# Performance work log

Measured on AMD Instinct MI355X. Metric: run time of the kernel, lower is better.

Reference implementation:

```python
import jax, jax.numpy as jnp
import numpy as np
import math

B, QL, HID = 1, 512, 4096
NH, NKV, HD = 32, 8, 128
PAST = 3584
THETA = 10000.0
GS = 32            # group_size for both K (k_bits=4 -> stays 32) and V
KBITS = 4
VBITS = 4
KRR = 0.125        # k_residual_ratio
VRR = 0.125        # v_residual_ratio


def qdq(x, g, bits):
    # asymmetric per-group quantize->dequantize along last dim (KVmix quantize_pack + dequant gemm)
    shp = x.shape
    xg = x.reshape(shp[:-1] + (shp[-1] // g, g))
    mn = xg.min(-1, keepdims=True)
    mx = xg.max(-1, keepdims=True)
    qmax = float(2 ** bits - 1)
    scale = (mx - mn) / qmax
    q = jnp.clip(jnp.round(jnp.where(scale > 0, (xg - mn) / jnp.where(scale > 0, scale, 1.0), 0.0)), 0.0, qmax)
    return (q * scale + mn).reshape(shp)


def _rope(x, cos, sin):
    h = x.shape[-1] // 2
    rot = jnp.concatenate([-x[..., h:], x[..., :h]], -1)
    return x * cos + rot * sin


def setup_inputs() -> dict:
    key = jax.random.key(0)
    ks = jax.random.split(key, 7)
    s = 0.02
    return {
        "hidden_states": jax.random.normal(ks[0], (B, QL, HID), jnp.float32),
        "past_key": jax.random.normal(ks[1], (B, NKV, PAST, HD), jnp.float32),
        "past_value": jax.random.normal(ks[2], (B, NKV, PAST, HD), jnp.float32),
        "wq": jax.random.normal(ks[3], (NH * HD, HID), jnp.float32) * s,
        "wk": jax.random.normal(ks[4], (NKV * HD, HID), jnp.float32) * s,
        "wv": jax.random.normal(ks[5], (NKV * HD, HID), jnp.float32) * s,
        "wo": jax.random.normal(ks[6], (HID, NH * HD), jnp.float32) * s,
        "position_ids": (jnp.arange(QL, dtype=jnp.int32) + PAST)[None, :],
    }


def reference(hidden_states, past_key, past_value, wq, wk, wv, wo, position_ids):
    b, ql, _ = hidden_states.shape
    past_len = past_key.shape[2]
    kv_len = past_len + ql

    # projections -> [b, heads, seq, hd]
    q = (hidden_states @ wq.T).reshape(b, ql, NH, HD).transpose(0, 2, 1, 3)
    k = (hidden_states @ wk.T).reshape(b, ql, NKV, HD).transpose(0, 2, 1, 3)
    v = (hidden_states @ wv.T).reshape(b, ql, NKV, HD).transpose(0, 2, 1, 3)

    # rotary embedding (HF Mistral style)
    inv_freq = 1.0 / (THETA ** (jnp.arange(0, HD, 2, dtype=jnp.float32) / HD))
    freqs = position_ids.astype(jnp.float32)[..., None] * inv_freq       # [b, ql, hd/2]
    emb = jnp.concatenate([freqs, freqs], -1)                            # [b, ql, hd]
    cos = jnp.cos(emb)[:, None]
    sin = jnp.sin(emb)[:, None]
    q = _rope(q, cos, sin)
    k = _rope(k, cos, sin)

    key_full = jnp.concatenate([past_key, k], axis=2)                    # [b, nkv, kv, hd]
    val_full = jnp.concatenate([past_value, v], axis=2)

    # residual split (static python ints)
    k_res = int(KRR * kv_len)
    kq_len = (kv_len - k_res) // GS * GS
    v_res = int(VRR * kv_len)
    vq_len = (kv_len - v_res) // GS * GS

    # K quantized along seq dim (transpose(2,3) then group last dim), V along head_dim
    key_q = qdq(key_full[:, :, :kq_len, :].transpose(0, 1, 3, 2), GS, KBITS)  # [b,nkv,hd,kq]
    key_f = key_full[:, :, kq_len:, :]
    val_q = qdq(val_full[:, :, :vq_len, :], GS, VBITS)
    val_f = val_full[:, :, vq_len:, :]

    rep = NH // NKV
    rkv = lambda x: jnp.repeat(x, rep, axis=1)

    att_q = jnp.einsum('bhqd,bhdk->bhqk', q, rkv(key_q))
    att_f = jnp.einsum('bhqd,bhkd->bhqk', q, rkv(key_f))
    attn = jnp.concatenate([att_q, att_f], -1).astype(jnp.float32) / math.sqrt(HD)

    qpos = past_len + jnp.arange(ql)
    mask = jnp.where(jnp.arange(kv_len)[None, :] <= qpos[:, None], 0.0, -1e30)
    attn = jax.nn.softmax(attn + mask, axis=-1)

    out = jnp.einsum('bhqk,bhkd->bhqd', attn[..., :vq_len], rkv(val_q)) \
        + jnp.einsum('bhqk,bhkd->bhqd', attn[..., vq_len:], rkv(val_f))
    out = out.transpose(0, 2, 1, 3).reshape(b, ql, NH * HD)
    return out @ wo.T
```

## Files before the change

kernel.cpp:

```cpp
#include <hip/hip_runtime.h>
#include <hip/hip_bf16.h>

typedef __bf16 bf16_t;
typedef __bf16 bf16x4 __attribute__((ext_vector_type(4)));
typedef __bf16 bf16x8 __attribute__((ext_vector_type(8)));
typedef float  f32x4  __attribute__((ext_vector_type(4)));

static __device__ __forceinline__ f32x4 mfma16(bf16x8 a, bf16x8 b, f32x4 c) {
  return __builtin_amdgcn_mfma_f32_16x16x32_bf16(a, b, c, 0, 0, 0);
}

typedef const __attribute__((address_space(1))) void* gas_t;
typedef __attribute__((address_space(3))) void* las_t;
#define ASYNC16(g, l) __builtin_amdgcn_global_load_lds((gas_t)(g), (las_t)(l), 16, 0, 0)

#define QL_   512
#define HID_  4096
#define NH_   32
#define NKV_  8
#define HD_   128
#define PAST_ 3584
#define KVL_  4096
#define NSPLIT 6

#define QSCALE 0.12751750152134056f

__global__ __launch_bounds__(256) void cvt_f32_bf16(
    const float* __restrict__ src, bf16_t* __restrict__ dst, int n4)
{
  int i = blockIdx.x * 256 + threadIdx.x;
  const int stride = gridDim.x * 256;
  for (; i < n4; i += stride) {
    float4 f = ((const float4*)src)[i];
    bf16x4 o;
    o[0] = (bf16_t)f.x; o[1] = (bf16_t)f.y; o[2] = (bf16_t)f.z; o[3] = (bf16_t)f.w;
    ((bf16x4*)dst)[i] = o;
  }
}

template<bool C_F32>
__global__ __launch_bounds__(256) void gemm_bt(
    const bf16_t* __restrict__ A,
    const bf16_t* __restrict__ B0, const bf16_t* __restrict__ B1,
    const bf16_t* __restrict__ B2, int nsplit1, int nsplit2,
    void* __restrict__ Cptr, int K, int lda, int ldb, int ldc)
{
  constexpr int BM = 128, BN = 64, BK = 32;
  __shared__ bf16_t As[BM * BK];
  __shared__ bf16_t Bs[BN * BK];

  const int tid = threadIdx.x;
  const int w = tid >> 6, lane = tid & 63;
  const int lm = lane & 15, quad = lane >> 4;
  const int wr = w >> 1, wc = w & 1;
  const int bm0 = blockIdx.y * BM, bn0 = blockIdx.x * BN;

  const bf16_t* Bseg; int bn_loc;
  if (bn0 < nsplit1)      { Bseg = B0; bn_loc = bn0; }
  else if (bn0 < nsplit2) { Bseg = B1; bn_loc = bn0 - nsplit1; }
  else                    { Bseg = B2; bn_loc = bn0 - nsplit2; }

  int rA[2], cA[2];
#pragma unroll
  for (int j = 0; j < 2; j++) {
    const int g = (w * 2 + j) * 64 + lane;
    rA[j] = g >> 2;
    cA[j] = (g & 3) ^ ((rA[j] >> 1) & 3);
  }
  const int gB = w * 64 + lane;
  const int rB = gB >> 2;
  const int cB = (gB & 3) ^ ((rB >> 1) & 3);

  f32x4 acc[4][2];
#pragma unroll
  for (int i = 0; i < 4; i++)
#pragma unroll
    for (int j = 0; j < 2; j++) acc[i][j] = f32x4{0.f, 0.f, 0.f, 0.f};

  const bf16_t* Abase = A + (size_t)bm0 * lda;
  const bf16_t* Bbase = Bseg + (size_t)bn_loc * ldb;

  for (int k0 = 0; k0 < K; k0 += BK) {
    ASYNC16(Abase + (size_t)rA[0] * lda + k0 + cA[0] * 8, &As[(w * 2 + 0) * 512]);
    ASYNC16(Abase + (size_t)rA[1] * lda + k0 + cA[1] * 8, &As[(w * 2 + 1) * 512]);
    ASYNC16(Bbase + (size_t)rB * ldb + k0 + cB * 8,       &Bs[w * 512]);
    __syncthreads();

    bf16x8 af[4], bfr[2];
#pragma unroll
    for (int mt = 0; mt < 4; mt++) {
      const int r = wr * 64 + mt * 16 + lm;
      af[mt] = *(const bf16x8*)&As[(r * 4 + (quad ^ ((r >> 1) & 3))) * 8];
    }
#pragma unroll
    for (int nt = 0; nt < 2; nt++) {
      const int r = wc * 32 + nt * 16 + lm;
      bfr[nt] = *(const bf16x8*)&Bs[(r * 4 + (quad ^ ((r >> 1) & 3))) * 8];
    }
#pragma unroll
    for (int mt = 0; mt < 4; mt++)
#pragma unroll
      for (int nt = 0; nt < 2; nt++)
        acc[mt][nt] = mfma16(af[mt], bfr[nt], acc[mt][nt]);
    __syncthreads();
  }

#pragma unroll
  for (int mt = 0; mt < 4; mt++) {
#pragma unroll
    for (int nt = 0; nt < 2; nt++) {
      const int row = bm0 + wr * 64 + mt * 16 + quad * 4;
      const int col = bn0 + wc * 32 + nt * 16 + lm;
#pragma unroll
      for (int r = 0; r < 4; r++) {
        if constexpr (C_F32)
          ((float*)Cptr)[(size_t)(row + r) * ldc + col] = acc[mt][nt][r];
        else
          ((bf16_t*)Cptr)[(size_t)(row + r) * ldc + col] = (bf16_t)acc[mt][nt][r];
      }
    }
  }
}

__global__ __launch_bounds__(128) void dequant_key(
    const float* __restrict__ pk, bf16_t* __restrict__ Kf)
{
  const int g = blockIdx.x, h = blockIdx.y, d = threadIdx.x;
  const float* src = pk + ((size_t)h * PAST_ + g * 32) * HD_ + d;
  float x[32];
  float mn = 1e30f, mx = -1e30f;
#pragma unroll
  for (int s = 0; s < 32; s++) {
    x[s] = src[(size_t)s * HD_];
    mn = fminf(mn, x[s]); mx = fmaxf(mx, x[s]);
  }
  float scale = (mx - mn) / 15.0f;
  bf16_t* dst = Kf + ((size_t)h * KVL_ + g * 32) * HD_ + d;
#pragma unroll
  for (int s = 0; s < 32; s++) {
    float t = scale > 0.f ? (x[s] - mn) / scale : 0.f;
    float q = fminf(fmaxf(rintf(t), 0.f), 15.f);
    dst[(size_t)s * HD_] = (bf16_t)(q * scale + mn);
  }
}

__global__ __launch_bounds__(256) void dequant_value(
    const float* __restrict__ pv, bf16_t* __restrict__ Vt)
{
  const int sc = blockIdx.x, h = blockIdx.y;
  const int j = threadIdx.x >> 6, lane = threadIdx.x & 63;
  const int s = sc * 64 + lane;
  const float* src = pv + ((size_t)h * PAST_ + s) * HD_ + j * 32;
  float x[32];
  float mn = 1e30f, mx = -1e30f;
#pragma unroll
  for (int q4 = 0; q4 < 8; q4++) {
    float4 f = ((const float4*)src)[q4];
    x[q4*4+0] = f.x; x[q4*4+1] = f.y; x[q4*4+2] = f.z; x[q4*4+3] = f.w;
    mn = fminf(fminf(mn, fminf(f.x, f.y)), fminf(f.z, f.w));
    mx = fmaxf(fmaxf(mx, fmaxf(f.x, f.y)), fmaxf(f.z, f.w));
  }
  float scale = (mx - mn) / 15.0f;
  bf16_t* dst = Vt + ((size_t)h * HD_ + j * 32) * KVL_ + s;
#pragma unroll
  for (int d = 0; d < 32; d++) {
    float t = scale > 0.f ? (x[d] - mn) / scale : 0.f;
    float q = fminf(fmaxf(rintf(t), 0.f), 15.f);
    dst[(size_t)d * KVL_] = (bf16_t)(q * scale + mn);
  }
}

__global__ __launch_bounds__(128) void rope_scatter(
    const bf16_t* __restrict__ Y, const int* __restrict__ posids,
    bf16_t* __restrict__ Qa, bf16_t* __restrict__ Kf, bf16_t* __restrict__ Vt)
{
  const int i = blockIdx.x;
  const int u = blockIdx.y;
  const int d = threadIdx.x;

  if (u >= 40) {
    const int hv = u - 40;
    float v = (float)Y[(size_t)i * 6144 + 5120 + hv * HD_ + d];
    Vt[((size_t)hv * HD_ + d) * KVL_ + PAST_ + i] = (bf16_t)v;
    return;
  }
  const int pos = posids[i];
  const int fi = d & 63;
  const float inv_freq = exp2f(-(float)fi * 0.2076205059304601f);
  const float ang = (float)pos * inv_freq;
  float sn, cs;
  sincosf(ang, &sn, &cs);

  if (u < 32) {
    const bf16_t* src = &Y[(size_t)i * 6144 + u * HD_];
    float x  = (float)src[d];
    float xo = (float)src[d ^ 64];
    float rot = (d < 64) ? -xo : xo;
    Qa[((size_t)u * QL_ + i) * HD_ + d] = (bf16_t)((x * cs + rot * sn) * QSCALE);
  } else {
    const int hk = u - 32;
    const bf16_t* src = &Y[(size_t)i * 6144 + 4096 + hk * HD_];
    float x  = (float)src[d];
    float xo = (float)src[d ^ 64];
    float rot = (d < 64) ? -xo : xo;
    Kf[((size_t)hk * KVL_ + PAST_ + i) * HD_ + d] = (bf16_t)(x * cs + rot * sn);
  }
}

__global__ __launch_bounds__(256, 3) void attn_kernel(
    const bf16_t* __restrict__ Qa, const bf16_t* __restrict__ Kf,
    const bf16_t* __restrict__ Vt, bf16_t* __restrict__ Opart,
    float* __restrict__ ML)
{
  __shared__ bf16_t Ks[64 * 128];
  __shared__ bf16_t Vts[144 * 64];
  __shared__ bf16_t Pw[4 * 32 * 64];

  const int tid = threadIdx.x, w = tid >> 6, lane = tid & 63;
  const int lm = lane & 15, quad = lane >> 4;
  const int qt = blockIdx.x, h = blockIdx.y, sp = blockIdx.z;
  const int kvh = h >> 2;
  const int qw = qt * 128 + w * 32;

  if (tid < 64) Vts[128 * 64 + tid] = (bf16_t)1.0f;

  bf16x8 qf[2][4];
#pragma unroll
  for (int mt = 0; mt < 2; mt++)
#pragma unroll
    for (int kb = 0; kb < 4; kb++)
      qf[mt][kb] = *(const bf16x8*)&Qa[((size_t)h * QL_ + qw + mt * 16 + lm) * HD_ + kb * 32 + quad * 8];

  f32x4 o[2][8], ol[2];
#pragma unroll
  for (int mt = 0; mt < 2; mt++) {
    ol[mt] = f32x4{0.f, 0.f, 0.f, 0.f};
#pragma unroll
    for (int i = 0; i < 8; i++) o[mt][i] = f32x4{0.f, 0.f, 0.f, 0.f};
  }

  int offK[4], offV[4], sid_[4];
#pragma unroll
  for (int j = 0; j < 4; j++) {
    const int sid = (w * 4 + j) * 64 + lane;
    sid_[j] = sid;
    const int kr = sid >> 4, ksp = sid & 15;
    offK[j] = kr * HD_ + (ksp ^ (kr & 7)) * 8;
    const int vr = sid >> 3, vsp = sid & 7;
    offV[j] = vr * KVL_ + (vsp ^ (vr & 7)) * 8;
  }
  const bf16_t* Kbase = Kf + (size_t)kvh * KVL_ * HD_;
  const bf16_t* Vbase = Vt + (size_t)kvh * HD_ * KVL_;

  const int T = 58 + 2 * qt;
  const int t0 = sp * T / NSPLIT;
  const int t1 = (sp + 1) * T / NSPLIT;

  for (int it = t0; it < t1; ++it) {
    const int kv0 = it * 64;
#pragma unroll
    for (int j = 0; j < 4; j++)
      ASYNC16(Kbase + (size_t)kv0 * HD_ + offK[j], &Ks[sid_[j] * 8]);
#pragma unroll
    for (int j = 0; j < 4; j++)
      ASYNC16(Vbase + kv0 + offV[j], &Vts[sid_[j] * 8]);
    __syncthreads();

    const bool needmask = (it >= T - 2);

#pragma unroll
    for (int nt = 0; nt < 4; nt++) {
      const int krow = nt * 16 + lm;
      f32x4 s0 = f32x4{0.f, 0.f, 0.f, 0.f};
      f32x4 s1 = f32x4{0.f, 0.f, 0.f, 0.f};
#pragma unroll
      for (int kb = 0; kb < 4; kb++) {
        bf16x8 kfrag = *(const bf16x8*)&Ks[krow * 128 + (((kb * 4 + quad) ^ (lm & 7)) * 8)];
        s0 = mfma16(qf[0][kb], kfrag, s0);
        s1 = mfma16(qf[1][kb], kfrag, s1);
      }
      if (needmask) {
        const int col = kv0 + nt * 16 + lm;
#pragma unroll
        for (int r = 0; r < 4; r++) {
          if (col > PAST_ + qw + quad * 4 + r)      s0[r] = -1e30f;
          if (col > PAST_ + qw + 16 + quad * 4 + r) s1[r] = -1e30f;
        }
      }
#pragma unroll
      for (int r = 0; r < 4; r++) {
        const int row0 = quad * 4 + r;
        const int sp0 = ((nt * 2) + (lm >> 3)) ^ (row0 & 7);
        Pw[(w * 32 + row0) * 64 + sp0 * 8 + (lm & 7)] = (bf16_t)exp2f(s0[r]);
        const int row1 = 16 + quad * 4 + r;
        const int sp1 = ((nt * 2) + (lm >> 3)) ^ (row1 & 7);
        Pw[(w * 32 + row1) * 64 + sp1 * 8 + (lm & 7)] = (bf16_t)exp2f(s1[r]);
      }
    }

    bf16x8 pf[2][2];
#pragma unroll
    for (int mt = 0; mt < 2; mt++)
#pragma unroll
      for (int kb = 0; kb < 2; kb++)
        pf[mt][kb] = *(const bf16x8*)&Pw[(w * 32 + mt * 16 + lm) * 64 + (((kb * 4 + quad) ^ (lm & 7)) * 8)];
#pragma unroll
    for (int dt = 0; dt < 8; dt++) {
      const int vrow = dt * 16 + lm;
#pragma unroll
      for (int kb = 0; kb < 2; kb++) {
        bf16x8 vf = *(const bf16x8*)&Vts[vrow * 64 + (((kb * 4 + quad) ^ (lm & 7)) * 8)];
        o[0][dt] = mfma16(pf[0][kb], vf, o[0][dt]);
        o[1][dt] = mfma16(pf[1][kb], vf, o[1][dt]);
      }
    }
    {
      const int vrow = 128 + lm;
#pragma unroll
      for (int kb = 0; kb < 2; kb++) {
        bf16x8 vf = *(const bf16x8*)&Vts[vrow * 64 + (((kb * 4 + quad) ^ (lm & 7)) * 8)];
        ol[0] = mfma16(pf[0][kb], vf, ol[0]);
        ol[1] = mfma16(pf[1][kb], vf, ol[1]);
      }
    }
    __syncthreads();
  }

  const size_t pbase = ((size_t)(sp * NH_ + h) * QL_ + qw);
#pragma unroll
  for (int mt = 0; mt < 2; mt++) {
#pragma unroll
    for (int dt = 0; dt < 8; dt++)
#pragma unroll
      for (int r = 0; r < 4; r++)
        Opart[(pbase + mt * 16 + quad * 4 + r) * HD_ + dt * 16 + lm] = (bf16_t)o[mt][dt][r];
  }
  if (lm == 0) {
#pragma unroll
    for (int mt = 0; mt < 2; mt++)
#pragma unroll
      for (int r = 0; r < 4; r++)
        ML[pbase + mt * 16 + quad * 4 + r] = ol[mt][r];
  }
}

__global__ __launch_bounds__(128) void combine_kernel(
    const bf16_t* __restrict__ Opart, const float* __restrict__ ML,
    bf16_t* __restrict__ AttnO)
{
  const int q = blockIdx.x, h = blockIdx.y, d = threadIdx.x;
  float lsum = 0.f, o = 0.f;
#pragma unroll
  for (int s = 0; s < NSPLIT; s++) {
    const size_t base = (size_t)(s * NH_ + h) * QL_ + q;
    lsum += ML[base];
    o += (float)Opart[base * HD_ + d];
  }
  AttnO[(size_t)q * (NH_ * HD_) + h * HD_ + d] = (bf16_t)(o / lsum);
}

extern "C" void kernel_launch(void* const* d_in, const int* in_sizes, int n_in,
                              void* d_out, int out_size, void* d_ws, size_t ws_size,
                              hipStream_t stream)
{
  (void)in_sizes; (void)n_in; (void)out_size; (void)ws_size;
  const float* hidden = (const float*)d_in[0];
  const float* past_k = (const float*)d_in[1];
  const float* past_v = (const float*)d_in[2];
  const float* wq  = (const float*)d_in[3];
  const float* wk  = (const float*)d_in[4];
  const float* wv  = (const float*)d_in[5];
  const float* wo  = (const float*)d_in[6];
  const int*   pos = (const int*)d_in[7];

  char* p = (char*)d_ws;
  bf16_t* Y     = (bf16_t*)p;  p += (size_t)QL_ * 6144 * 2;
  bf16_t* Qa    = (bf16_t*)p;  p += (size_t)QL_ * NH_ * HD_ * 2;
  bf16_t* Kf    = (bf16_t*)p;  p += (size_t)NKV_ * KVL_ * HD_ * 2;
  bf16_t* Vt    = (bf16_t*)p;  p += (size_t)NKV_ * HD_ * KVL_ * 2;
  bf16_t* AttnO = (bf16_t*)p;  p += (size_t)QL_ * NH_ * HD_ * 2;
  bf16_t* Opart = (bf16_t*)p;  p += (size_t)NSPLIT * NH_ * QL_ * HD_ * 2;
  float*  ML    = (float*)p;   p += (size_t)NSPLIT * NH_ * QL_ * 4;
  bf16_t* Hbf   = (bf16_t*)p;  p += (size_t)QL_ * HID_ * 2;
  bf16_t* Wbuf  = (bf16_t*)p;  p += (size_t)4096 * HID_ * 2;
  bf16_t* Wkbf  = (bf16_t*)p;  p += (size_t)1024 * HID_ * 2;
  bf16_t* Wvbf  = (bf16_t*)p;  p += (size_t)1024 * HID_ * 2;

  const int CVB = 1024;
  cvt_f32_bf16<<<CVB, 256, 0, stream>>>(hidden, Hbf,  QL_ * HID_ / 4);
  cvt_f32_bf16<<<CVB, 256, 0, stream>>>(wq, Wbuf, 4096 * HID_ / 4);
  cvt_f32_bf16<<<CVB, 256, 0, stream>>>(wk, Wkbf, 1024 * HID_ / 4);
  cvt_f32_bf16<<<CVB, 256, 0, stream>>>(wv, Wvbf, 1024 * HID_ / 4);
  dequant_key  <<<dim3(PAST_ / 32, NKV_), dim3(128), 0, stream>>>(past_k, Kf);
  dequant_value<<<dim3(PAST_ / 64, NKV_), dim3(256), 0, stream>>>(past_v, Vt);

  gemm_bt<false><<<dim3(6144 / 64, QL_ / 128), dim3(256), 0, stream>>>(
      Hbf, Wbuf, Wkbf, Wvbf, 4096, 5120, (void*)Y, HID_, HID_, HID_, 6144);

  cvt_f32_bf16<<<CVB, 256, 0, stream>>>(wo, Wbuf, HID_ * 4096 / 4);

  rope_scatter<<<dim3(QL_, 48), dim3(128), 0, stream>>>(Y, pos, Qa, Kf, Vt);
  attn_kernel <<<dim3(QL_ / 128, NH_, NSPLIT), dim3(256), 0, stream>>>(Qa, Kf, Vt, Opart, ML);
  combine_kernel<<<dim3(QL_, NH_), dim3(128), 0, stream>>>(Opart, ML, AttnO);

  gemm_bt<true><<<dim3(4096 / 64, QL_ / 128), dim3(256), 0, stream>>>(
      AttnO, Wbuf, Wbuf, Wbuf, 1 << 30, 1 << 30, d_out,
      NH_ * HD_, NH_ * HD_, HID_, HID_);
}
```

Before: 466.2 us.

## Store K/V in MFMA fragment order, read directly from global, double-buffer GEMM

Dequant and rope kernels now write K and V in a layout that matches the MFMA operand fragments, so the attention kernel loads them straight from global memory (L2) into registers with no LDS staging or per-tile barriers. The row-sum now uses a constant ones vector instead of an extra LDS row. The attention grid is flattened to a 1D index that groups heads sharing a KV head, and NSPLIT drops from 6 to 4. The projection GEMMs switch to 64x64x64 tiles with double-buffered async LDS loads. The trade-off is reliance on cache for K/V reuse across heads in place of shared memory, and smaller GEMM tiles that reload more data.

```diff
diff --git a/kernel.cpp b/kernel.cpp
--- a/kernel.cpp
+++ b/kernel.cpp
@@ -21,9 +21,18 @@
 #define HD_   128
 #define PAST_ 3584
 #define KVL_  4096
-#define NSPLIT 6
+#define NSPLIT 4
 
 #define QSCALE 0.12751750152134056f
+
+static __device__ __forceinline__ size_t kidx(int s, int d) {
+  return ((size_t)(((s >> 6) * 4 + ((s >> 4) & 3)) * 4 + (d >> 5))) * 512
+         + ((((d >> 3) & 3) * 16 + (s & 15)) * 8) + (d & 7);
+}
+static __device__ __forceinline__ size_t vidx(int s, int d) {
+  return ((size_t)(((s >> 6) * 8 + (d >> 4)) * 2 + ((s >> 5) & 1))) * 512
+         + (((((s >> 3) & 3) * 16 + (d & 15)) * 8)) + (s & 7);
+}
 
 __global__ __launch_bounds__(256) void cvt_f32_bf16(
     const float* __restrict__ src, bf16_t* __restrict__ dst, int n4)
@@ -45,9 +54,9 @@
     const bf16_t* __restrict__ B2, int nsplit1, int nsplit2,
     void* __restrict__ Cptr, int K, int lda, int ldb, int ldc)
 {
-  constexpr int BM = 128, BN = 64, BK = 32;
-  __shared__ bf16_t As[BM * BK];
-  __shared__ bf16_t Bs[BN * BK];
+  constexpr int BM = 64, BN = 64, BK = 64;
+  __shared__ bf16_t As[2][BM * BK];
+  __shared__ bf16_t Bs[2][BN * BK];
 
   const int tid = threadIdx.x;
   const int w = tid >> 6, lane = tid & 63;
@@ -60,56 +69,67 @@
   else if (bn0 < nsplit2) { Bseg = B1; bn_loc = bn0 - nsplit1; }
   else                    { Bseg = B2; bn_loc = bn0 - nsplit2; }
 
-  int rA[2], cA[2];
+  int sid[2], soff[2];
 #pragma unroll
   for (int j = 0; j < 2; j++) {
-    const int g = (w * 2 + j) * 64 + lane;
-    rA[j] = g >> 2;
-    cA[j] = (g & 3) ^ ((rA[j] >> 1) & 3);
-  }
-  const int gB = w * 64 + lane;
-  const int rB = gB >> 2;
-  const int cB = (gB & 3) ^ ((rB >> 1) & 3);
-
-  f32x4 acc[4][2];
-#pragma unroll
-  for (int i = 0; i < 4; i++)
-#pragma unroll
-    for (int j = 0; j < 2; j++) acc[i][j] = f32x4{0.f, 0.f, 0.f, 0.f};
-
+    sid[j] = j * 256 + tid;
+    const int r = sid[j] >> 3, c = sid[j] & 7;
+    soff[j] = r * 64 + (c ^ (r & 7)) * 8;
+  }
   const bf16_t* Abase = A + (size_t)bm0 * lda;
   const bf16_t* Bbase = Bseg + (size_t)bn_loc * ldb;
 
+  f32x4 acc[2][2];
+#pragma unroll
+  for (int i = 0; i < 2; i++)
+#pragma unroll
+    for (int j = 0; j < 2; j++) acc[i][j] = f32x4{0.f, 0.f, 0.f, 0.f};
+
+#pragma unroll
+  for (int j = 0; j < 2; j++) {
+    const int r = soff[j] >> 6, c = soff[j] & 63;
+    ASYNC16(Abase + (size_t)r * lda + c, &As[0][sid[j] * 8]);
+    ASYNC16(Bbase + (size_t)r * ldb + c, &Bs[0][sid[j] * 8]);
+  }
+
+  int cur = 0;
   for (int k0 = 0; k0 < K; k0 += BK) {
-    ASYNC16(Abase + (size_t)rA[0] * lda + k0 + cA[0] * 8, &As[(w * 2 + 0) * 512]);
-    ASYNC16(Abase + (size_t)rA[1] * lda + k0 + cA[1] * 8, &As[(w * 2 + 1) * 512]);
-    ASYNC16(Bbase + (size_t)rB * ldb + k0 + cB * 8,       &Bs[w * 512]);
     __syncthreads();
-
-    bf16x8 af[4], bfr[2];
-#pragma unroll
-    for (int mt = 0; mt < 4; mt++) {
-      const int r = wr * 64 + mt * 16 + lm;
-      af[mt] = *(const bf16x8*)&As[(r * 4 + (quad ^ ((r >> 1) & 3))) * 8];
-    }
+    if (k0 + BK < K) {
+#pragma unroll
+      for (int j = 0; j < 2; j++) {
+        const int r = soff[j] >> 6, c = soff[j] & 63;
+        ASYNC16(Abase + (size_t)r * lda + k0 + BK + c, &As[cur ^ 1][sid[j] * 8]);
+        ASYNC16(Bbase + (size_t)r * ldb + k0 + BK + c, &Bs[cur ^ 1][sid[j] * 8]);
+      }
+    }
+#pragma unroll
+    for (int kb = 0; kb < 2; kb++) {
+      bf16x8 af[2], bf[2];
+#pragma unroll
+      for (int mt = 0; mt < 2; mt++) {
+        const int r = wr * 32 + mt * 16 + lm;
+        af[mt] = *(const bf16x8*)&As[cur][r * 64 + (((kb * 4 + quad) ^ (r & 7)) * 8)];
+      }
+#pragma unroll
+      for (int nt = 0; nt < 2; nt++) {
+        const int r = wc * 32 + nt * 16 + lm;
+        bf[nt] = *(const bf16x8*)&Bs[cur][r * 64 + (((kb * 4 + quad) ^ (r & 7)) * 8)];
+      }
+#pragma unroll
+      for (int mt = 0; mt < 2; mt++)
+#pragma unroll
+        for (int nt = 0; nt < 2; nt++)
+          acc[mt][nt] = mfma16(af[mt], bf[nt], acc[mt][nt]);
+    }
+    cur ^= 1;
+  }
+
+#pragma unroll
+  for (int mt = 0; mt < 2; mt++) {
 #pragma unroll
     for (int nt = 0; nt < 2; nt++) {
-      const int r = wc * 32 + nt * 16 + lm;
-      bfr[nt] = *(const bf16x8*)&Bs[(r * 4 + (quad ^ ((r >> 1) & 3))) * 8];
-    }
-#pragma unroll
-    for (int mt = 0; mt < 4; mt++)
-#pragma unroll
-      for (int nt = 0; nt < 2; nt++)
-        acc[mt][nt] = mfma16(af[mt], bfr[nt], acc[mt][nt]);
-    __syncthreads();
-  }
-
-#pragma unroll
-  for (int mt = 0; mt < 4; mt++) {
-#pragma unroll
-    for (int nt = 0; nt < 2; nt++) {
-      const int row = bm0 + wr * 64 + mt * 16 + quad * 4;
+      const int row = bm0 + wr * 32 + mt * 16 + quad * 4;
       const int col = bn0 + wc * 32 + nt * 16 + lm;
 #pragma unroll
       for (int r = 0; r < 4; r++) {
@@ -123,7 +143,7 @@
 }
 
 __global__ __launch_bounds__(128) void dequant_key(
-    const float* __restrict__ pk, bf16_t* __restrict__ Kf)
+    const float* __restrict__ pk, bf16_t* __restrict__ Kc)
 {
   const int g = blockIdx.x, h = blockIdx.y, d = threadIdx.x;
   const float* src = pk + ((size_t)h * PAST_ + g * 32) * HD_ + d;
@@ -135,17 +155,17 @@
     mn = fminf(mn, x[s]); mx = fmaxf(mx, x[s]);
   }
   float scale = (mx - mn) / 15.0f;
-  bf16_t* dst = Kf + ((size_t)h * KVL_ + g * 32) * HD_ + d;
+  bf16_t* dst = Kc + (size_t)h * (KVL_ * HD_);
 #pragma unroll
   for (int s = 0; s < 32; s++) {
     float t = scale > 0.f ? (x[s] - mn) / scale : 0.f;
     float q = fminf(fmaxf(rintf(t), 0.f), 15.f);
-    dst[(size_t)s * HD_] = (bf16_t)(q * scale + mn);
+    dst[kidx(g * 32 + s, d)] = (bf16_t)(q * scale + mn);
   }
 }
 
 __global__ __launch_bounds__(256) void dequant_value(
-    const float* __restrict__ pv, bf16_t* __restrict__ Vt)
+    const float* __restrict__ pv, bf16_t* __restrict__ Vc)
 {
   const int sc = blockIdx.x, h = blockIdx.y;
   const int j = threadIdx.x >> 6, lane = threadIdx.x & 63;
@@ -161,18 +181,18 @@
     mx = fmaxf(fmaxf(mx, fmaxf(f.x, f.y)), fmaxf(f.z, f.w));
   }
   float scale = (mx - mn) / 15.0f;
-  bf16_t* dst = Vt + ((size_t)h * HD_ + j * 32) * KVL_ + s;
+  bf16_t* dst = Vc + (size_t)h * (KVL_ * HD_);
 #pragma unroll
   for (int d = 0; d < 32; d++) {
     float t = scale > 0.f ? (x[d] - mn) / scale : 0.f;
     float q = fminf(fmaxf(rintf(t), 0.f), 15.f);
-    dst[(size_t)d * KVL_] = (bf16_t)(q * scale + mn);
+    dst[vidx(s, j * 32 + d)] = (bf16_t)(q * scale + mn);
   }
 }
 
 __global__ __launch_bounds__(128) void rope_scatter(
     const bf16_t* __restrict__ Y, const int* __restrict__ posids,
-    bf16_t* __restrict__ Qa, bf16_t* __restrict__ Kf, bf16_t* __restrict__ Vt)
+    bf16_t* __restrict__ Qa, bf16_t* __restrict__ Kc, bf16_t* __restrict__ Vc)
 {
   const int i = blockIdx.x;
   const int u = blockIdx.y;
@@ -181,7 +201,7 @@
   if (u >= 40) {
     const int hv = u - 40;
     float v = (float)Y[(size_t)i * 6144 + 5120 + hv * HD_ + d];
-    Vt[((size_t)hv * HD_ + d) * KVL_ + PAST_ + i] = (bf16_t)v;
+    Vc[(size_t)hv * (KVL_ * HD_) + vidx(PAST_ + i, d)] = (bf16_t)v;
     return;
   }
   const int pos = posids[i];
@@ -203,26 +223,30 @@
     float x  = (float)src[d];
     float xo = (float)src[d ^ 64];
     float rot = (d < 64) ? -xo : xo;
-    Kf[((size_t)hk * KVL_ + PAST_ + i) * HD_ + d] = (bf16_t)(x * cs + rot * sn);
+    Kc[(size_t)hk * (KVL_ * HD_) + kidx(PAST_ + i, d)] = (bf16_t)(x * cs + rot * sn);
   }
 }
 
 __global__ __launch_bounds__(256, 3) void attn_kernel(
-    const bf16_t* __restrict__ Qa, const bf16_t* __restrict__ Kf,
-    const bf16_t* __restrict__ Vt, bf16_t* __restrict__ Opart,
+    const bf16_t* __restrict__ Qa, const bf16_t* __restrict__ Kc,
+    const bf16_t* __restrict__ Vc, bf16_t* __restrict__ Opart,
     float* __restrict__ ML)
 {
-  __shared__ bf16_t Ks[64 * 128];
-  __shared__ bf16_t Vts[144 * 64];
-  __shared__ bf16_t Pw[4 * 32 * 64];
+  __shared__ bf16_t Pw[4][32 * 64];
 
   const int tid = threadIdx.x, w = tid >> 6, lane = tid & 63;
   const int lm = lane & 15, quad = lane >> 4;
-  const int qt = blockIdx.x, h = blockIdx.y, sp = blockIdx.z;
-  const int kvh = h >> 2;
+  const int idx = blockIdx.x;
+  const int grp = idx & 31;
+  const int inner = idx >> 5;
+  const int sp = grp >> 3, kvh = grp & 7;
+  const int h = kvh * 4 + (inner & 3);
+  const int qt = inner >> 2;
   const int qw = qt * 128 + w * 32;
 
-  if (tid < 64) Vts[128 * 64 + tid] = (bf16_t)1.0f;
+  bf16x8 ones8;
+#pragma unroll
+  for (int j = 0; j < 8; j++) ones8[j] = (bf16_t)1.0f;
 
   bf16x8 qf[2][4];
 #pragma unroll
@@ -239,45 +263,28 @@
     for (int i = 0; i < 8; i++) o[mt][i] = f32x4{0.f, 0.f, 0.f, 0.f};
   }
 
-  int offK[4], offV[4], sid_[4];
-#pragma unroll
-  for (int j = 0; j < 4; j++) {
-    const int sid = (w * 4 + j) * 64 + lane;
-    sid_[j] = sid;
-    const int kr = sid >> 4, ksp = sid & 15;
-    offK[j] = kr * HD_ + (ksp ^ (kr & 7)) * 8;
-    const int vr = sid >> 3, vsp = sid & 7;
-    offV[j] = vr * KVL_ + (vsp ^ (vr & 7)) * 8;
-  }
-  const bf16_t* Kbase = Kf + (size_t)kvh * KVL_ * HD_;
-  const bf16_t* Vbase = Vt + (size_t)kvh * HD_ * KVL_;
+  const bf16_t* Kb = Kc + (size_t)kvh * (KVL_ * HD_);
+  const bf16_t* Vb = Vc + (size_t)kvh * (KVL_ * HD_);
 
   const int T = 58 + 2 * qt;
   const int t0 = sp * T / NSPLIT;
   const int t1 = (sp + 1) * T / NSPLIT;
 
   for (int it = t0; it < t1; ++it) {
+    const bf16_t* kt = Kb + (size_t)it * 8192;
+    const bf16_t* vt = Vb + (size_t)it * 8192;
+    const bool needmask = (it >= T - 2);
     const int kv0 = it * 64;
-#pragma unroll
-    for (int j = 0; j < 4; j++)
-      ASYNC16(Kbase + (size_t)kv0 * HD_ + offK[j], &Ks[sid_[j] * 8]);
-#pragma unroll
-    for (int j = 0; j < 4; j++)
-      ASYNC16(Vbase + kv0 + offV[j], &Vts[sid_[j] * 8]);
-    __syncthreads();
-
-    const bool needmask = (it >= T - 2);
 
 #pragma unroll
     for (int nt = 0; nt < 4; nt++) {
-      const int krow = nt * 16 + lm;
       f32x4 s0 = f32x4{0.f, 0.f, 0.f, 0.f};
       f32x4 s1 = f32x4{0.f, 0.f, 0.f, 0.f};
 #pragma unroll
       for (int kb = 0; kb < 4; kb++) {
-        bf16x8 kfrag = *(const bf16x8*)&Ks[krow * 128 + (((kb * 4 + quad) ^ (lm & 7)) * 8)];
-        s0 = mfma16(qf[0][kb], kfrag, s0);
-        s1 = mfma16(qf[1][kb], kfrag, s1);
+        bf16x8 kf = *(const bf16x8*)&kt[((nt * 4 + kb) * 64 + lane) * 8];
+        s0 = mfma16(qf[0][kb], kf, s0);
+        s1 = mfma16(qf[1][kb], kf, s1);
       }
       if (needmask) {
         const int col = kv0 + nt * 16 + lm;
@@ -290,11 +297,11 @@
 #pragma unroll
       for (int r = 0; r < 4; r++) {
         const int row0 = quad * 4 + r;
-        const int sp0 = ((nt * 2) + (lm >> 3)) ^ (row0 & 7);
-        Pw[(w * 32 + row0) * 64 + sp0 * 8 + (lm & 7)] = (bf16_t)exp2f(s0[r]);
+        const int sg0 = ((nt * 2) + (lm >> 3)) ^ (row0 & 7);
+        Pw[w][row0 * 64 + sg0 * 8 + (lm & 7)] = (bf16_t)exp2f(s0[r]);
         const int row1 = 16 + quad * 4 + r;
-        const int sp1 = ((nt * 2) + (lm >> 3)) ^ (row1 & 7);
-        Pw[(w * 32 + row1) * 64 + sp1 * 8 + (lm & 7)] = (bf16_t)exp2f(s1[r]);
+        const int sg1 = ((nt * 2) + (lm >> 3)) ^ (row1 & 7);
+        Pw[w][row1 * 64 + sg1 * 8 + (lm & 7)] = (bf16_t)exp2f(s1[r]);
       }
     }
 
@@ -302,28 +309,24 @@
 #pragma unroll
     for (int mt = 0; mt < 2; mt++)
 #pragma unroll
-      for (int kb = 0; kb < 2; kb++)
-        pf[mt][kb] = *(const bf16x8*)&Pw[(w * 32 + mt * 16 + lm) * 64 + (((kb * 4 + quad) ^ (lm & 7)) * 8)];
+      for (int kb = 0; kb < 2; kb++) {
+        const int r = mt * 16 + lm;
+        pf[mt][kb] = *(const bf16x8*)&Pw[w][r * 64 + (((kb * 4 + quad) ^ (r & 7)) * 8)];
+      }
 #pragma unroll
     for (int dt = 0; dt < 8; dt++) {
-      const int vrow = dt * 16 + lm;
 #pragma unroll
       for (int kb = 0; kb < 2; kb++) {
-        bf16x8 vf = *(const bf16x8*)&Vts[vrow * 64 + (((kb * 4 + quad) ^ (lm & 7)) * 8)];
+        bf16x8 vf = *(const bf16x8*)&vt[((dt * 2 + kb) * 64 + lane) * 8];
         o[0][dt] = mfma16(pf[0][kb], vf, o[0][dt]);
         o[1][dt] = mfma16(pf[1][kb], vf, o[1][dt]);
       }
     }
-    {
-      const int vrow = 128 + lm;
-#pragma unroll
-      for (int kb = 0; kb < 2; kb++) {
-        bf16x8 vf = *(const bf16x8*)&Vts[vrow * 64 + (((kb * 4 + quad) ^ (lm & 7)) * 8)];
-        ol[0] = mfma16(pf[0][kb], vf, ol[0]);
-        ol[1] = mfma16(pf[1][kb], vf, ol[1]);
-      }
-    }
-    __syncthreads();
+#pragma unroll
+    for (int kb = 0; kb < 2; kb++) {
+      ol[0] = mfma16(pf[0][kb], ones8, ol[0]);
+      ol[1] = mfma16(pf[1][kb], ones8, ol[1]);
+    }
   }
 
   const size_t pbase = ((size_t)(sp * NH_ + h) * QL_ + qw);
@@ -376,8 +379,8 @@
   char* p = (char*)d_ws;
   bf16_t* Y     = (bf16_t*)p;  p += (size_t)QL_ * 6144 * 2;
   bf16_t* Qa    = (bf16_t*)p;  p += (size_t)QL_ * NH_ * HD_ * 2;
-  bf16_t* Kf    = (bf16_t*)p;  p += (size_t)NKV_ * KVL_ * HD_ * 2;
-  bf16_t* Vt    = (bf16_t*)p;  p += (size_t)NKV_ * HD_ * KVL_ * 2;
+  bf16_t* Kc    = (bf16_t*)p;  p += (size_t)NKV_ * KVL_ * HD_ * 2;
+  bf16_t* Vc    = (bf16_t*)p;  p += (size_t)NKV_ * HD_ * KVL_ * 2;
   bf16_t* AttnO = (bf16_t*)p;  p += (size_t)QL_ * NH_ * HD_ * 2;
   bf16_t* Opart = (bf16_t*)p;  p += (size_t)NSPLIT * NH_ * QL_ * HD_ * 2;
   float*  ML    = (float*)p;   p += (size_t)NSPLIT * NH_ * QL_ * 4;
@@ -391,19 +394,19 @@
   cvt_f32_bf16<<<CVB, 256, 0, stream>>>(wq, Wbuf, 4096 * HID_ / 4);
   cvt_f32_bf16<<<CVB, 256, 0, stream>>>(wk, Wkbf, 1024 * HID_ / 4);
   cvt_f32_bf16<<<CVB, 256, 0, stream>>>(wv, Wvbf, 1024 * HID_ / 4);
-  dequant_key  <<<dim3(PAST_ / 32, NKV_), dim3(128), 0, stream>>>(past_k, Kf);
-  dequant_value<<<dim3(PAST_ / 64, NKV_), dim3(256), 0, stream>>>(past_v, Vt);
-
-  gemm_bt<false><<<dim3(6144 / 64, QL_ / 128), dim3(256), 0, stream>>>(
+  dequant_key  <<<dim3(PAST_ / 32, NKV_), dim3(128), 0, stream>>>(past_k, Kc);
+  dequant_value<<<dim3(PAST_ / 64, NKV_), dim3(256), 0, stream>>>(past_v, Vc);
+
+  gemm_bt<false><<<dim3(6144 / 64, QL_ / 64), dim3(256), 0, stream>>>(
       Hbf, Wbuf, Wkbf, Wvbf, 4096, 5120, (void*)Y, HID_, HID_, HID_, 6144);
 
   cvt_f32_bf16<<<CVB, 256, 0, stream>>>(wo, Wbuf, HID_ * 4096 / 4);
 
-  rope_scatter<<<dim3(QL_, 48), dim3(128), 0, stream>>>(Y, pos, Qa, Kf, Vt);
-  attn_kernel <<<dim3(QL_ / 128, NH_, NSPLIT), dim3(256), 0, stream>>>(Qa, Kf, Vt, Opart, ML);
+  rope_scatter<<<dim3(QL_, 48), dim3(128), 0, stream>>>(Y, pos, Qa, Kc, Vc);
+  attn_kernel <<<dim3(16 * 32), dim3(256), 0, stream>>>(Qa, Kc, Vc, Opart, ML);
   combine_kernel<<<dim3(QL_, NH_), dim3(128), 0, stream>>>(Opart, ML, AttnO);
 
-  gemm_bt<true><<<dim3(4096 / 64, QL_ / 128), dim3(256), 0, stream>>>(
+  gemm_bt<true><<<dim3(4096 / 64, QL_ / 64), dim3(256), 0, stream>>>(
       AttnO, Wbuf, Wbuf, Wbuf, 1 << 30, 1 << 30, d_out,
       NH_ * HD_, NH_ * HD_, HID_, HID_);
 }
```

Result: faster. 444.0 us (-4.8%).
